# Optimization experiments

Hardware: AMD Instinct MI355X
Metric: run time of the kernel (lower is better)

The kernel has to match this reference:

```python
import jax, jax.numpy as jnp
import numpy as np

NUM_HEADS = 16

def setup_inputs() -> dict:
    key = jax.random.key(0)
    ks = jax.random.split(key, 5)
    E = 1024
    x = jax.random.normal(ks[0], (2, 2048, E), dtype=jnp.float32)
    w_in = jax.random.normal(ks[1], (3 * E, E), dtype=jnp.float32) * (E ** -0.5)
    b_in = jax.random.normal(ks[2], (3 * E,), dtype=jnp.float32) * 0.02
    w_out = jax.random.normal(ks[3], (E, E), dtype=jnp.float32) * (E ** -0.5)
    b_out = jax.random.normal(ks[4], (E,), dtype=jnp.float32) * 0.02
    return {"x": x, "w_in": w_in, "b_in": b_in, "w_out": w_out, "b_out": b_out}


def reference(x, w_in, b_in, w_out, b_out):
    B, N, E = x.shape
    H = NUM_HEADS
    Dh = E // H
    # fused QKV projection (torch Linear: x @ W^T + b)
    qkv = x @ w_in.T + b_in                      # [B, N, 3E]
    q, k, v = jnp.split(qkv, 3, axis=-1)
    # [B, H, N, Dh]
    q = q.reshape(B, N, H, Dh).transpose(0, 2, 1, 3)
    k = k.reshape(B, N, H, Dh).transpose(0, 2, 1, 3)
    v = v.reshape(B, N, H, Dh).transpose(0, 2, 1, 3)
    scale = Dh ** -0.5
    scores = jnp.einsum("bhqd,bhkd->bhqk", q, k) * scale  # [B, H, N, N]
    attn = jax.nn.softmax(scores, axis=-1)
    out = jnp.einsum("bhqk,bhkd->bhqd", attn, v)          # [B, H, N, Dh]
    out = out.transpose(0, 2, 1, 3).reshape(B, N, E)
    return out @ w_out.T + b_out
```

## Files before the change

### kernel.cpp

```cpp
#include <hip/hip_runtime.h>


typedef __bf16 bf16;
typedef __bf16 bf16x8 __attribute__((ext_vector_type(8)));
typedef __bf16 bf16x4 __attribute__((ext_vector_type(4)));
typedef float  f32x4  __attribute__((ext_vector_type(4)));

#define MFMA16(a, b, c) __builtin_amdgcn_mfma_f32_16x16x32_bf16((a), (b), (c), 0, 0, 0)

#define SC2 0.18033688011112042f

__device__ __forceinline__ void gld_lds16(const void* g, void* l) {
  __builtin_amdgcn_global_load_lds((const __attribute__((address_space(1))) void*)g,
                                   (__attribute__((address_space(3))) void*)l,
                                   16, 0, 0);
}

__global__ __launch_bounds__(256) void cast3_kernel(
    const float* __restrict__ x, const float* __restrict__ wi,
    const float* __restrict__ wo, bf16* __restrict__ xb,
    bf16* __restrict__ wib, bf16* __restrict__ wob) {
  const int i = (blockIdx.x * 256 + threadIdx.x) * 4;
  const float* s; bf16* d; int off;
  if (i < 4194304)      { s = x;  d = xb;  off = i; }
  else if (i < 7340032) { s = wi; d = wib; off = i - 4194304; }
  else                  { s = wo; d = wob; off = i - 7340032; }
  const float4 v = *(const float4*)(s + off);
  bf16x4 o;
  o[0] = (bf16)v.x; o[1] = (bf16)v.y; o[2] = (bf16)v.z; o[3] = (bf16)v.w;
  *(bf16x4*)(d + off) = o;
}

__global__ __launch_bounds__(256) void gemm_qkv_kernel(
    const bf16* __restrict__ A,
    const bf16* __restrict__ B,
    const float* __restrict__ bias,
    bf16* __restrict__ qb, bf16* __restrict__ kb, bf16* __restrict__ vb) {
  constexpr int K = 1024;
  __shared__ __align__(16) char smem[128 * 136 * 2];
  bf16* As = (bf16*)smem;
  bf16* Bs = (bf16*)(smem + 8192);
  const int tid  = threadIdx.x;
  const int lane = tid & 63;
  const int wave = tid >> 6;
  const int m0 = blockIdx.y * 128;
  const int n0 = blockIdx.x * 128;
  const int r_ = tid >> 2;
  const int k_ = (tid & 3) * 8;
  const int lr = lane & 15, lg = lane >> 4;
  const int wm = (wave >> 1) * 64, wn = (wave & 1) * 64;

  f32x4 acc[4][4];
#pragma unroll
  for (int i = 0; i < 4; ++i)
#pragma unroll
    for (int j = 0; j < 4; ++j) acc[i][j] = (f32x4){0.f, 0.f, 0.f, 0.f};

  for (int k0 = 0; k0 < K; k0 += 32) {
    __syncthreads();
    gld_lds16(A + (size_t)(m0 + r_) * K + k0 + k_,      (char*)As + tid * 16);
    gld_lds16(A + (size_t)(m0 + 64 + r_) * K + k0 + k_, (char*)As + 4096 + tid * 16);
    gld_lds16(B + (size_t)(n0 + r_) * K + k0 + k_,      (char*)Bs + tid * 16);
    gld_lds16(B + (size_t)(n0 + 64 + r_) * K + k0 + k_, (char*)Bs + 4096 + tid * 16);
    __syncthreads();

    bf16x8 af[4], bfr[4];
#pragma unroll
    for (int i = 0; i < 4; ++i)
      af[i] = *(const bf16x8*)((const char*)As + (size_t)((wm + i * 16 + lr) * 32 + lg * 8) * 2);
#pragma unroll
    for (int j = 0; j < 4; ++j)
      bfr[j] = *(const bf16x8*)((const char*)Bs + (size_t)((wn + j * 16 + lr) * 32 + lg * 8) * 2);
#pragma unroll
    for (int i = 0; i < 4; ++i)
#pragma unroll
      for (int j = 0; j < 4; ++j) acc[i][j] = MFMA16(af[i], bfr[j], acc[i][j]);
  }

  if (n0 < 2048) {
    const int isq = (n0 < 1024);
#pragma unroll
    for (int j = 0; j < 4; ++j) {
      const int col = n0 + wn + j * 16 + lr;
      const float bv = bias[col];
      const int wi = col & 1023;
      const int h = wi >> 6, d = wi & 63;
      bf16* dst = isq ? qb : kb;
      const float scl = isq ? SC2 : 1.0f;
#pragma unroll
      for (int i = 0; i < 4; ++i) {
#pragma unroll
        for (int r = 0; r < 4; ++r) {
          const int row = m0 + wm + i * 16 + lg * 4 + r;
          const int bb = row >> 11, nn = row & 2047;
          dst[((size_t)(bb * 16 + h) * 2048 + nn) * 64 + d] =
              (bf16)((acc[i][j][r] + bv) * scl);
        }
      }
    }
  } else {
    __syncthreads();
    bf16* Vt = (bf16*)smem;
#pragma unroll
    for (int j = 0; j < 4; ++j) {
      const int c = wn + j * 16 + lr;
      const float bv = bias[n0 + c];
#pragma unroll
      for (int i = 0; i < 4; ++i) {
#pragma unroll
        for (int r = 0; r < 4; ++r) {
          const int rr = wm + i * 16 + lg * 4 + r;
          Vt[c * 136 + rr] = (bf16)(acc[i][j][r] + bv);
        }
      }
    }
    __syncthreads();
    const int wi0 = n0 - 2048;
    const int bb = m0 >> 11, nn0 = m0 & 2047;
#pragma unroll
    for (int pass = 0; pass < 8; ++pass) {
      const int c = pass * 16 + (tid >> 4);
      const int nof = (tid & 15) * 8;
      const int wi = wi0 + c;
      const int h = wi >> 6, d = wi & 63;
      *(bf16x8*)(vb + ((size_t)(bb * 16 + h) * 64 + d) * 2048 + nn0 + nof) =
          *(const bf16x8*)(Vt + c * 136 + nof);
    }
  }
}

__global__ __launch_bounds__(256) void flash_attn_kernel(
    const bf16* __restrict__ q, const bf16* __restrict__ k,
    const bf16* __restrict__ vt, bf16* __restrict__ o) {
  __shared__ bf16 Ks[2][64 * 64];
  __shared__ bf16 Vs[2][64 * 64];
  __shared__ bf16 Pl[4][2][16 * 72];

  const int tid  = threadIdx.x;
  const int lane = tid & 63;
  const int wave = tid >> 6;
  const int lr = lane & 15, lg = lane >> 4;
  const int qt = blockIdx.x;
  const int bh = blockIdx.y;
  const bf16* qp = q  + (size_t)bh * (2048 * 64);
  const bf16* kp = k  + (size_t)bh * (2048 * 64);
  const bf16* vp = vt + (size_t)bh * (64 * 2048);
  const int q0 = qt * 128 + wave * 32;

  int srow[2], scol[2];
#pragma unroll
  for (int p = 0; p < 2; ++p) {
    const int L = p * 4096 + tid * 16;
    srow[p] = L >> 7;
    scol[p] = ((L & 127) ^ ((srow[p] & 7) << 4)) >> 1;
  }

  bf16x8 qf[2][2];
#pragma unroll
  for (int qi = 0; qi < 2; ++qi)
#pragma unroll
    for (int t = 0; t < 2; ++t)
      qf[qi][t] = *(const bf16x8*)(qp + (size_t)(q0 + qi * 16 + lr) * 64 + t * 32 + lg * 8);

  bf16x8 ones;
#pragma unroll
  for (int i = 0; i < 8; ++i) ones[i] = (bf16)1.0f;

  f32x4 oacc[2][4];
#pragma unroll
  for (int qi = 0; qi < 2; ++qi)
#pragma unroll
    for (int j = 0; j < 4; ++j) oacc[qi][j] = (f32x4){0.f, 0.f, 0.f, 0.f};
  f32x4 lacc[2];
#pragma unroll
  for (int qi = 0; qi < 2; ++qi) lacc[qi] = (f32x4){0.f, 0.f, 0.f, 0.f};

#pragma unroll
  for (int p = 0; p < 2; ++p) {
    const int L = p * 4096 + tid * 16;
    gld_lds16(kp + (size_t)srow[p] * 64 + scol[p],       (char*)Ks[0] + L);
    gld_lds16(vp + (size_t)srow[p] * 2048 + 0 + scol[p], (char*)Vs[0] + L);
  }
  __syncthreads();

  int buf = 0;
  for (int t = 0; t < 32; ++t) {
    if (t + 1 < 32) {
      const int nkv = t * 64 + 64;
#pragma unroll
      for (int p = 0; p < 2; ++p) {
        const int L = p * 4096 + tid * 16;
        gld_lds16(kp + (size_t)(nkv + srow[p]) * 64 + scol[p], (char*)Ks[buf ^ 1] + L);
        gld_lds16(vp + (size_t)srow[p] * 2048 + nkv + scol[p], (char*)Vs[buf ^ 1] + L);
      }
    }

    f32x4 s[2][4];
#pragma unroll
    for (int qi = 0; qi < 2; ++qi)
#pragma unroll
      for (int sub = 0; sub < 4; ++sub) s[qi][sub] = (f32x4){0.f, 0.f, 0.f, 0.f};
    __builtin_amdgcn_s_setprio(1);
#pragma unroll
    for (int sub = 0; sub < 4; ++sub) {
#pragma unroll
      for (int tt = 0; tt < 2; ++tt) {
        const int row = sub * 16 + lr;
        const int byte = (row << 7) + (((tt * 32 + lg * 8) << 1) ^ ((row & 7) << 4));
        bf16x8 kf = *(const bf16x8*)((const char*)Ks[buf] + byte);
#pragma unroll
        for (int qi = 0; qi < 2; ++qi) s[qi][sub] = MFMA16(kf, qf[qi][tt], s[qi][sub]);
      }
    }
    __builtin_amdgcn_s_setprio(0);

#pragma unroll
    for (int qi = 0; qi < 2; ++qi) {
      bf16* pl = &Pl[wave][qi][0];
#pragma unroll
      for (int sub = 0; sub < 4; ++sub) {
        const float e0 = exp2f(s[qi][sub][0]);
        const float e1 = exp2f(s[qi][sub][1]);
        const float e2 = exp2f(s[qi][sub][2]);
        const float e3 = exp2f(s[qi][sub][3]);
        unsigned p01, p23;
        asm("v_cvt_pk_bf16_f32 %0, %1, %2" : "=v"(p01) : "v"(e0), "v"(e1));
        asm("v_cvt_pk_bf16_f32 %0, %1, %2" : "=v"(p23) : "v"(e2), "v"(e3));
        uint2 w; w.x = p01; w.y = p23;
        *(uint2*)(pl + lr * 72 + sub * 16 + lg * 4) = w;
      }
    }
    bf16x8 pa[2][2];
#pragma unroll
    for (int qi = 0; qi < 2; ++qi)
#pragma unroll
      for (int kk = 0; kk < 2; ++kk)
        pa[qi][kk] = *(const bf16x8*)(&Pl[wave][qi][0] + lr * 72 + kk * 32 + lg * 8);

    __builtin_amdgcn_s_setprio(1);
#pragma unroll
    for (int j = 0; j < 4; ++j) {
#pragma unroll
      for (int kk = 0; kk < 2; ++kk) {
        const int row = j * 16 + lr;
        const int byte = (row << 7) + (((kk * 32 + lg * 8) << 1) ^ ((row & 7) << 4));
        bf16x8 vf = *(const bf16x8*)((const char*)Vs[buf] + byte);
#pragma unroll
        for (int qi = 0; qi < 2; ++qi) oacc[qi][j] = MFMA16(pa[qi][kk], vf, oacc[qi][j]);
      }
    }
#pragma unroll
    for (int qi = 0; qi < 2; ++qi)
#pragma unroll
      for (int kk = 0; kk < 2; ++kk)
        lacc[qi] = MFMA16(pa[qi][kk], ones, lacc[qi]);
    __builtin_amdgcn_s_setprio(0);

    __syncthreads();
    buf ^= 1;
  }

  const int b = bh >> 4, h = bh & 15;
#pragma unroll
  for (int qi = 0; qi < 2; ++qi) {
    float inv[4];
#pragma unroll
    for (int r = 0; r < 4; ++r) inv[r] = 1.f / lacc[qi][r];
#pragma unroll
    for (int j = 0; j < 4; ++j) {
#pragma unroll
      for (int r = 0; r < 4; ++r) {
        const int qrow = q0 + qi * 16 + lg * 4 + r;
        o[((size_t)(b * 2048 + qrow)) * 1024 + h * 64 + j * 16 + lr] =
            (bf16)(oacc[qi][j][r] * inv[r]);
      }
    }
  }
}

__global__ __launch_bounds__(256) void gemm_out_kernel(
    const bf16* __restrict__ A,
    const bf16* __restrict__ B,
    const float* __restrict__ bias,
    float* __restrict__ out) {
  constexpr int K = 1024;
  __shared__ bf16 As[128 * 32];
  __shared__ bf16 Bs[128 * 32];
  const int tid  = threadIdx.x;
  const int lane = tid & 63;
  const int wave = tid >> 6;
  const int m0 = blockIdx.y * 128;
  const int n0 = blockIdx.x * 128;
  const int r_ = tid >> 2;
  const int k_ = (tid & 3) * 8;
  const int lr = lane & 15, lg = lane >> 4;
  const int wm = (wave >> 1) * 64, wn = (wave & 1) * 64;

  f32x4 acc[4][4];
#pragma unroll
  for (int i = 0; i < 4; ++i)
#pragma unroll
    for (int j = 0; j < 4; ++j) acc[i][j] = (f32x4){0.f, 0.f, 0.f, 0.f};

  for (int k0 = 0; k0 < K; k0 += 32) {
    __syncthreads();
    gld_lds16(A + (size_t)(m0 + r_) * K + k0 + k_,      (char*)As + tid * 16);
    gld_lds16(A + (size_t)(m0 + 64 + r_) * K + k0 + k_, (char*)As + 4096 + tid * 16);
    gld_lds16(B + (size_t)(n0 + r_) * K + k0 + k_,      (char*)Bs + tid * 16);
    gld_lds16(B + (size_t)(n0 + 64 + r_) * K + k0 + k_, (char*)Bs + 4096 + tid * 16);
    __syncthreads();

    bf16x8 af[4], bfr[4];
#pragma unroll
    for (int i = 0; i < 4; ++i)
      af[i] = *(const bf16x8*)((const char*)As + (size_t)((wm + i * 16 + lr) * 32 + lg * 8) * 2);
#pragma unroll
    for (int j = 0; j < 4; ++j)
      bfr[j] = *(const bf16x8*)((const char*)Bs + (size_t)((wn + j * 16 + lr) * 32 + lg * 8) * 2);
#pragma unroll
    for (int i = 0; i < 4; ++i)
#pragma unroll
      for (int j = 0; j < 4; ++j) acc[i][j] = MFMA16(af[i], bfr[j], acc[i][j]);
  }

#pragma unroll
  for (int j = 0; j < 4; ++j) {
    const int col = n0 + wn + j * 16 + lr;
    const float bv = bias[col];
#pragma unroll
    for (int i = 0; i < 4; ++i) {
#pragma unroll
      for (int r = 0; r < 4; ++r) {
        const int row = m0 + wm + i * 16 + lg * 4 + r;
        out[(size_t)row * 1024 + col] = acc[i][j][r] + bv;
      }
    }
  }
}

extern "C" void kernel_launch(void* const* d_in, const int* in_sizes, int n_in,
                              void* d_out, int out_size, void* d_ws, size_t ws_size,
                              hipStream_t stream) {
  const float* x     = (const float*)d_in[0];
  const float* w_in  = (const float*)d_in[1];
  const float* b_in  = (const float*)d_in[2];
  const float* w_out = (const float*)d_in[3];
  const float* b_out = (const float*)d_in[4];
  float* out = (float*)d_out;

  char* ws = (char*)d_ws;
  const size_t MB = 1ull << 20;
  bf16* xb  = (bf16*)(ws + 0 * MB);
  bf16* wib = (bf16*)(ws + 8 * MB);
  bf16* wob = (bf16*)(ws + 14 * MB);
  bf16* qb  = (bf16*)(ws + 16 * MB);
  bf16* kb  = (bf16*)(ws + 24 * MB);
  bf16* vb  = (bf16*)(ws + 32 * MB);
  bf16* ab  = (bf16*)(ws + 40 * MB);

  cast3_kernel<<<dim3(8192), dim3(256), 0, stream>>>(x, w_in, w_out, xb, wib, wob);
  gemm_qkv_kernel<<<dim3(24, 32), dim3(256), 0, stream>>>(xb, wib, b_in, qb, kb, vb);
  flash_attn_kernel<<<dim3(16, 32), dim3(256), 0, stream>>>(qb, kb, vb, ab);
  gemm_out_kernel<<<dim3(8, 32), dim3(256), 0, stream>>>(ab, wob, b_out, out);
}
```

Measured before the change: 219.6 us.

## Stage Q/K epilogue through LDS for coalesced stores; swizzle P tile, raw exp

The QKV GEMM epilogue for Q and K now writes the tile into shared memory and then emits 16-byte vector stores per row, instead of scattered 2-byte global stores. In the attention kernel, the padded P staging buffer is replaced by an XOR-swizzled 64-wide layout, which saves LDS and aims to avoid bank conflicts. exp2f is replaced by raw v_exp_f32. The cost is an extra LDS round trip and barrier in the GEMM epilogue, plus the raw exp no longer handling denormal or range edge cases.

```diff
diff --git a/kernel.cpp b/kernel.cpp
--- a/kernel.cpp
+++ b/kernel.cpp
@@ -14,6 +14,12 @@
   __builtin_amdgcn_global_load_lds((const __attribute__((address_space(1))) void*)g,
                                    (__attribute__((address_space(3))) void*)l,
                                    16, 0, 0);
+}
+
+__device__ __forceinline__ float exp2_raw(float x) {
+  float r;
+  asm("v_exp_f32 %0, %1" : "=v"(r) : "v"(x));
+  return r;
 }
 
 __global__ __launch_bounds__(256) void cast3_kernel(
@@ -77,54 +83,59 @@
       for (int j = 0; j < 4; ++j) acc[i][j] = MFMA16(af[i], bfr[j], acc[i][j]);
   }
 
-  if (n0 < 2048) {
-    const int isq = (n0 < 1024);
+  __syncthreads();
+  bf16* T = (bf16*)smem;
+  const int which = n0 >> 10;
+  const int wi0 = n0 & 1023;
+  const int bb = m0 >> 11, nn0 = m0 & 2047;
+
+  if (which < 2) {
+    const float scl = (which == 0) ? SC2 : 1.0f;
 #pragma unroll
     for (int j = 0; j < 4; ++j) {
-      const int col = n0 + wn + j * 16 + lr;
-      const float bv = bias[col];
-      const int wi = col & 1023;
-      const int h = wi >> 6, d = wi & 63;
-      bf16* dst = isq ? qb : kb;
-      const float scl = isq ? SC2 : 1.0f;
-#pragma unroll
-      for (int i = 0; i < 4; ++i) {
+      const int tcol = wn + j * 16 + lr;
+      const float bv = bias[n0 + tcol];
+#pragma unroll
+      for (int i = 0; i < 4; ++i)
 #pragma unroll
         for (int r = 0; r < 4; ++r) {
-          const int row = m0 + wm + i * 16 + lg * 4 + r;
-          const int bb = row >> 11, nn = row & 2047;
-          dst[((size_t)(bb * 16 + h) * 2048 + nn) * 64 + d] =
-              (bf16)((acc[i][j][r] + bv) * scl);
+          const int trow = wm + i * 16 + lg * 4 + r;
+          T[trow * 136 + tcol] = (bf16)((acc[i][j][r] + bv) * scl);
         }
-      }
+    }
+    __syncthreads();
+    bf16* dst = (which == 0) ? qb : kb;
+    const int l = tid & 15, g = tid >> 4;
+    const int cc = l * 8;
+    const int h = (wi0 + cc) >> 6, d = cc & 63;
+#pragma unroll
+    for (int p = 0; p < 8; ++p) {
+      const int rr = p * 16 + g;
+      *(bf16x8*)(dst + ((size_t)(bb * 16 + h) * 2048 + nn0 + rr) * 64 + d) =
+          *(const bf16x8*)(T + rr * 136 + cc);
     }
   } else {
-    __syncthreads();
-    bf16* Vt = (bf16*)smem;
 #pragma unroll
     for (int j = 0; j < 4; ++j) {
       const int c = wn + j * 16 + lr;
       const float bv = bias[n0 + c];
 #pragma unroll
-      for (int i = 0; i < 4; ++i) {
+      for (int i = 0; i < 4; ++i)
 #pragma unroll
         for (int r = 0; r < 4; ++r) {
           const int rr = wm + i * 16 + lg * 4 + r;
-          Vt[c * 136 + rr] = (bf16)(acc[i][j][r] + bv);
+          T[c * 136 + rr] = (bf16)(acc[i][j][r] + bv);
         }
-      }
-    }
-    __syncthreads();
-    const int wi0 = n0 - 2048;
-    const int bb = m0 >> 11, nn0 = m0 & 2047;
-#pragma unroll
-    for (int pass = 0; pass < 8; ++pass) {
-      const int c = pass * 16 + (tid >> 4);
-      const int nof = (tid & 15) * 8;
-      const int wi = wi0 + c;
-      const int h = wi >> 6, d = wi & 63;
+    }
+    __syncthreads();
+    const int l = tid & 15, g = tid >> 4;
+    const int nof = l * 8;
+#pragma unroll
+    for (int p = 0; p < 8; ++p) {
+      const int c = p * 16 + g;
+      const int h = (wi0 + c) >> 6, d = (wi0 + c) & 63;
       *(bf16x8*)(vb + ((size_t)(bb * 16 + h) * 64 + d) * 2048 + nn0 + nof) =
-          *(const bf16x8*)(Vt + c * 136 + nof);
+          *(const bf16x8*)(T + c * 136 + nof);
     }
   }
 }
@@ -134,7 +145,7 @@
     const bf16* __restrict__ vt, bf16* __restrict__ o) {
   __shared__ bf16 Ks[2][64 * 64];
   __shared__ bf16 Vs[2][64 * 64];
-  __shared__ bf16 Pl[4][2][16 * 72];
+  __shared__ bf16 Pl[4][2][16 * 64];
 
   const int tid  = threadIdx.x;
   const int lane = tid & 63;
@@ -146,6 +157,7 @@
   const bf16* kp = k  + (size_t)bh * (2048 * 64);
   const bf16* vp = vt + (size_t)bh * (64 * 2048);
   const int q0 = qt * 128 + wave * 32;
+  const int wmask = (lr & 7) << 4;
 
   int srow[2], scol[2];
 #pragma unroll
@@ -216,18 +228,18 @@
 
 #pragma unroll
     for (int qi = 0; qi < 2; ++qi) {
-      bf16* pl = &Pl[wave][qi][0];
+      char* pl = (char*)&Pl[wave][qi][0] + lr * 128;
 #pragma unroll
       for (int sub = 0; sub < 4; ++sub) {
-        const float e0 = exp2f(s[qi][sub][0]);
-        const float e1 = exp2f(s[qi][sub][1]);
-        const float e2 = exp2f(s[qi][sub][2]);
-        const float e3 = exp2f(s[qi][sub][3]);
+        const float e0 = exp2_raw(s[qi][sub][0]);
+        const float e1 = exp2_raw(s[qi][sub][1]);
+        const float e2 = exp2_raw(s[qi][sub][2]);
+        const float e3 = exp2_raw(s[qi][sub][3]);
         unsigned p01, p23;
         asm("v_cvt_pk_bf16_f32 %0, %1, %2" : "=v"(p01) : "v"(e0), "v"(e1));
         asm("v_cvt_pk_bf16_f32 %0, %1, %2" : "=v"(p23) : "v"(e2), "v"(e3));
         uint2 w; w.x = p01; w.y = p23;
-        *(uint2*)(pl + lr * 72 + sub * 16 + lg * 4) = w;
+        *(uint2*)(pl + ((sub * 32 + lg * 8) ^ wmask)) = w;
       }
     }
     bf16x8 pa[2][2];
@@ -235,7 +247,8 @@
     for (int qi = 0; qi < 2; ++qi)
 #pragma unroll
       for (int kk = 0; kk < 2; ++kk)
-        pa[qi][kk] = *(const bf16x8*)(&Pl[wave][qi][0] + lr * 72 + kk * 32 + lg * 8);
+        pa[qi][kk] = *(const bf16x8*)((const char*)&Pl[wave][qi][0] + lr * 128 +
+                                      ((kk * 64 + lg * 16) ^ wmask));
 
     __builtin_amdgcn_s_setprio(1);
 #pragma unroll
```

Result: faster. 204.9 us (-6.7%).
